# Kernel tuning notes

Hardware: AMD Instinct MI355X
Metric: run time of the kernel (lower is better)

The kernel has to match this reference:

```python
import jax, jax.numpy as jnp
import numpy as np

B, C_IN, L = 256, 4, 2048
HNODE, GLEN = 256, 24
SIGMA_CONV, SIGMA_NEU = 0.1, 0.1
DROPPROB = 0.5


def setup_inputs() -> dict:
    key = jax.random.key(0)
    ks = jax.random.split(key, 7)
    x = jax.random.normal(ks[0], (B, C_IN, L), dtype=jnp.float32)
    wConv = SIGMA_CONV * jax.random.normal(ks[1], (HNODE, C_IN, GLEN), dtype=jnp.float32)
    wRect = -jax.random.normal(ks[2], (HNODE,), dtype=jnp.float32)
    wHidden = 0.3 * jax.random.normal(ks[3], (2 * HNODE, 2 * HNODE), dtype=jnp.float32)
    wHiddenBias = 0.3 * jax.random.normal(ks[4], (2 * HNODE,), dtype=jnp.float32)
    wNeu = SIGMA_NEU * jax.random.normal(ks[5], (2 * HNODE, 1), dtype=jnp.float32)
    wNeuBias = SIGMA_NEU * jax.random.normal(ks[6], (1,), dtype=jnp.float32)
    return {"x": x, "wConv": wConv, "wRect": wRect, "wHidden": wHidden,
            "wHiddenBias": wHiddenBias, "wNeu": wNeu, "wNeuBias": wNeuBias}


def reference(x, wConv, wRect, wHidden, wHiddenBias, wNeu, wNeuBias):
    # conv1d, stride 1, no padding: [B, HNODE, L-GLEN+1]
    conv = jax.lax.conv_general_dilated(
        x, wConv, window_strides=(1,), padding='VALID',
        dimension_numbers=('NCH', 'OIH', 'NCH'))
    rect = jnp.maximum(conv + wRect[None, :, None], 0.0)  # bias + relu-clamp
    maxPool = jnp.max(rect, axis=2)   # [B, HNODE]
    avgPool = jnp.mean(rect, axis=2)  # [B, HNODE]
    pool = jnp.concatenate([maxPool, avgPool], axis=1)  # [B, 2*HNODE]
    hid = jnp.maximum(pool @ wHidden + wHiddenBias, 0.0)
    out = DROPPROB * (hid @ wNeu) + wNeuBias  # [B, 1]
    return out
```

## Files before the change

### kernel.cpp

```cpp
#include <hip/hip_runtime.h>
#include <stdint.h>

#define CIN   4
#define LEN   2048
#define HN    256
#define GL    24
#define LOUT  2025
#define XP    2080

typedef short  s16x8 __attribute__((ext_vector_type(8)));
typedef float  f32x4 __attribute__((ext_vector_type(4)));

__device__ float g_pool[256 * 512];

static __device__ __forceinline__ uint16_t f2bf(float f) {
    union { float f; uint32_t u; } v; v.f = f;
    uint32_t u = v.u;
    return (uint16_t)((u + 0x7FFFu + ((u >> 16) & 1u)) >> 16);
}

#define SEL4(D, i) \
    ({ uint4 fu_ = {(D)[(i)], (D)[(i)+1], (D)[(i)+2], (D)[(i)+3]}; \
       __builtin_bit_cast(s16x8, fu_); })

static __device__ __forceinline__ void loadW(
    uint32_t (&E)[3][8], uint32_t (&O)[3][8],
    const uint16_t* xs, const uint16_t* xs2, const int (&abase)[3], int j)
{
    #pragma unroll
    for (int ks = 0; ks < 3; ++ks) {
        const uint4 e0 = *(const uint4*)&xs [abase[ks] + 128 * j];
        const uint4 e1 = *(const uint4*)&xs [abase[ks] + 128 * j + 8];
        const uint4 o0 = *(const uint4*)&xs2[abase[ks] + 128 * j];
        const uint4 o1 = *(const uint4*)&xs2[abase[ks] + 128 * j + 8];
        E[ks][0]=e0.x; E[ks][1]=e0.y; E[ks][2]=e0.z; E[ks][3]=e0.w;
        E[ks][4]=e1.x; E[ks][5]=e1.y; E[ks][6]=e1.z; E[ks][7]=e1.w;
        O[ks][0]=o0.x; O[ks][1]=o0.y; O[ks][2]=o0.z; O[ks][3]=o0.w;
        O[ks][4]=o1.x; O[ks][5]=o1.y; O[ks][6]=o1.z; O[ks][7]=o1.w;
    }
}

static __device__ __forceinline__ void procW(
    const uint32_t (&E)[3][8], const uint32_t (&O)[3][8],
    const s16x8 (&bfrag)[2][3], const float (&negb)[2],
    bool tail, int q, float (&rawmax)[2], float (&sums)[2])
{
    const f32x4 fzero = {0.f, 0.f, 0.f, 0.f};
    #pragma unroll
    for (int p = 0; p < 8; ++p) {
        s16x8 a0, a1, a2;
        if ((p & 1) == 0) {
            a0 = SEL4(E[0], p/2); a1 = SEL4(E[1], p/2); a2 = SEL4(E[2], p/2);
        } else {
            a0 = SEL4(O[0], (p-1)/2); a1 = SEL4(O[1], (p-1)/2); a2 = SEL4(O[2], (p-1)/2);
        }
        f32x4 acc0, acc1;
        acc0 = __builtin_amdgcn_mfma_f32_16x16x32_bf16(a0, bfrag[0][0], fzero, 0, 0, 0);
        acc1 = __builtin_amdgcn_mfma_f32_16x16x32_bf16(a0, bfrag[1][0], fzero, 0, 0, 0);
        acc0 = __builtin_amdgcn_mfma_f32_16x16x32_bf16(a1, bfrag[0][1], acc0, 0, 0, 0);
        acc1 = __builtin_amdgcn_mfma_f32_16x16x32_bf16(a1, bfrag[1][1], acc1, 0, 0, 0);
        acc0 = __builtin_amdgcn_mfma_f32_16x16x32_bf16(a2, bfrag[0][2], acc0, 0, 0, 0);
        acc1 = __builtin_amdgcn_mfma_f32_16x16x32_bf16(a2, bfrag[1][2], acc1, 0, 0, 0);

        if (!tail) {
            #pragma unroll
            for (int s = 0; s < 2; ++s) {
                const f32x4 a = (s == 0) ? acc0 : acc1;
                float t0 = fmaxf(a[0], negb[s]), t1 = fmaxf(a[1], negb[s]);
                float t2 = fmaxf(a[2], negb[s]), t3 = fmaxf(a[3], negb[s]);
                sums[s] += (t0 + t1) + (t2 + t3);
                rawmax[s] = fmaxf(fmaxf(rawmax[s], a[0]), a[1]);
                rawmax[s] = fmaxf(fmaxf(rawmax[s], a[2]), a[3]);
            }
        } else {
            #pragma unroll
            for (int s = 0; s < 2; ++s) {
                const f32x4 a = (s == 0) ? acc0 : acc1;
                #pragma unroll
                for (int r = 0; r < 4; ++r) {
                    int tpos = p + 128 * 15 + 32 * q + 8 * r;
                    float t = (tpos < LOUT) ? fmaxf(a[r], negb[s])
                                            : negb[s];
                    sums[s]   += t;
                    rawmax[s]  = fmaxf(rawmax[s], t);
                }
            }
        }
    }
}

__global__ __launch_bounds__(512) __attribute__((amdgpu_waves_per_eu(2, 2)))
void conv_pool_kernel(
    const float* __restrict__ x, const float* __restrict__ wConv,
    const float* __restrict__ wRect)
{
    __shared__ uint16_t xs [CIN * XP + 8];
    __shared__ uint16_t xs2[CIN * XP + 8];

    const int tid  = threadIdx.x;
    const int b    = blockIdx.x;
    const int lane = tid & 63;
    const int wid  = tid >> 6;
    const int n    = lane & 15;
    const int q    = lane >> 4;

    const float* xb = x + (size_t)b * (CIN * LEN);
    #pragma unroll
    for (int it = 0; it < 4; ++it) {
        int i = (tid + it * 512) * 4;
        float4 v = *(const float4*)(xb + i);
        int c = i >> 11, off = i & 2047;
        uint64_t pk =  (uint64_t)f2bf(v.x)
                    | ((uint64_t)f2bf(v.y) << 16)
                    | ((uint64_t)f2bf(v.z) << 32)
                    | ((uint64_t)f2bf(v.w) << 48);
        *(uint64_t*)&xs[c * XP + off] = pk;
    }
    if (tid < 64) {
        int c = tid >> 4, o = (tid & 15) * 2;
        *(uint32_t*)&xs[c * XP + 2048 + o] = 0u;
    }
    if (tid < 4) *(uint32_t*)&xs[CIN * XP + tid * 2] = 0u;

    s16x8 bfrag[2][3];
    float negb[2];
    #pragma unroll
    for (int s = 0; s < 2; ++s) {
        int h = wid * 32 + s * 16 + n;
        negb[s] = -wRect[h];
        #pragma unroll
        for (int ks = 0; ks < 3; ++ks) {
            int jb = ks * 4 + q;
            const float* wp_ = wConv + h * (CIN * GL) + jb * 8;
            float4 w0 = *(const float4*)(wp_);
            float4 w1 = *(const float4*)(wp_ + 4);
            s16x8 f;
            f[0]=(short)f2bf(w0.x); f[1]=(short)f2bf(w0.y);
            f[2]=(short)f2bf(w0.z); f[3]=(short)f2bf(w0.w);
            f[4]=(short)f2bf(w1.x); f[5]=(short)f2bf(w1.y);
            f[6]=(short)f2bf(w1.z); f[7]=(short)f2bf(w1.w);
            bfrag[s][ks] = f;
        }
    }

    int abase[3];
    #pragma unroll
    for (int ks = 0; ks < 3; ++ks) {
        int jb = ks * 4 + q;
        int c = jb / 3, g0 = (jb % 3) * 8;
        abase[ks] = c * XP + g0 + 8 * n;
    }

    __syncthreads();

    {
        const uint32_t* s0 = (const uint32_t*)xs;
        uint32_t*       s1 = (uint32_t*)xs2;
        #pragma unroll 1
        for (int g = tid; g < (CIN * XP) / 8; g += 512) {
            uint4 a = *(const uint4*)&s0[4 * g];
            uint32_t nx = s0[4 * g + 4];
            uint4 r;
            r.x = __builtin_amdgcn_alignbit(a.y, a.x, 16);
            r.y = __builtin_amdgcn_alignbit(a.z, a.y, 16);
            r.z = __builtin_amdgcn_alignbit(a.w, a.z, 16);
            r.w = __builtin_amdgcn_alignbit(nx,  a.w, 16);
            *(uint4*)&s1[4 * g] = r;
        }
    }
    __syncthreads();

    float rawmax[2] = {-1e30f, -1e30f};
    float sums[2]   = {0.f, 0.f};

    uint32_t EA[3][8], OA[3][8], EB[3][8], OB[3][8];
    loadW(EA, OA, xs, xs2, abase, 0);
    #pragma unroll 1
    for (int jj = 0; jj < 16; jj += 2) {
        loadW(EB, OB, xs, xs2, abase, jj + 1);
        procW(EA, OA, bfrag, negb, false, q, rawmax, sums);
        loadW(EA, OA, xs, xs2, abase, (jj + 2 < 16) ? jj + 2 : 15);
        procW(EB, OB, bfrag, negb, (jj + 1 == 15), q, rawmax, sums);
    }

    #pragma unroll
    for (int s = 0; s < 2; ++s) {
        float m  = rawmax[s], sm = sums[s];
        m  = fmaxf(m, __shfl_xor(m, 16, 64));  sm += __shfl_xor(sm, 16, 64);
        m  = fmaxf(m, __shfl_xor(m, 32, 64));  sm += __shfl_xor(sm, 32, 64);
        if (q == 0) {
            int h = wid * 32 + s * 16 + n;
            float bia = -negb[s];
            g_pool[(size_t)b * 512 + h]       = fmaxf(m + bia, 0.f);
            g_pool[(size_t)b * 512 + 256 + h] = (sm + 2048.f * bia) * (1.0f / 2025.0f);
        }
    }
}

__global__ __launch_bounds__(256, 4) void mlp_kernel(
    const float* __restrict__ wH, const float* __restrict__ bH,
    const float* __restrict__ wNeu, const float* __restrict__ wNeuB,
    float* __restrict__ out)
{
    __shared__ float pl[8][512];

    const int tid = threadIdx.x;
    const int og  = blockIdx.x & 7;
    const int bg  = blockIdx.x >> 3;
    const int o   = og * 64 + (tid & 63);
    const int wv  = tid >> 6;

    const float* ps = g_pool + (size_t)bg * 8 * 512;
    #pragma unroll
    for (int it = 0; it < 4; ++it) {
        int i = (tid + it * 256) * 4;
        *(float4*)&pl[0][i] = *(const float4*)(ps + i);
    }
    __syncthreads();

    float acc0 = 0.f, acc1 = 0.f;
    const float* prow0 = &pl[wv * 2][0];
    const float* prow1 = &pl[wv * 2 + 1][0];
    #pragma unroll 4
    for (int i = 0; i < 512; i += 4) {
        float4 p0 = *(const float4*)(prow0 + i);
        float4 p1 = *(const float4*)(prow1 + i);
        float w0 = wH[(i + 0) * 512 + o];
        float w1 = wH[(i + 1) * 512 + o];
        float w2 = wH[(i + 2) * 512 + o];
        float w3 = wH[(i + 3) * 512 + o];
        acc0 = fmaf(p0.x, w0, acc0); acc0 = fmaf(p0.y, w1, acc0);
        acc0 = fmaf(p0.z, w2, acc0); acc0 = fmaf(p0.w, w3, acc0);
        acc1 = fmaf(p1.x, w0, acc1); acc1 = fmaf(p1.y, w1, acc1);
        acc1 = fmaf(p1.z, w2, acc1); acc1 = fmaf(p1.w, w3, acc1);
    }
    float hb  = bH[o];
    float wn  = wNeu[o];
    float v0  = fmaxf(acc0 + hb, 0.f) * wn;
    float v1  = fmaxf(acc1 + hb, 0.f) * wn;
    #pragma unroll
    for (int dlt = 1; dlt < 64; dlt <<= 1) {
        v0 += __shfl_xor(v0, dlt, 64);
        v1 += __shfl_xor(v1, dlt, 64);
    }
    if ((tid & 63) == 0) {
        int b0 = bg * 8 + wv * 2;
        float bias = (og == 0) ? wNeuB[0] : 0.f;
        atomicAdd(&out[b0],     0.5f * v0 + bias);
        atomicAdd(&out[b0 + 1], 0.5f * v1 + bias);
    }
}

extern "C" void kernel_launch(void* const* d_in, const int* in_sizes, int n_in,
                              void* d_out, int out_size, void* d_ws, size_t ws_size,
                              hipStream_t stream) {
    const float* x        = (const float*)d_in[0];
    const float* wConv    = (const float*)d_in[1];
    const float* wRect    = (const float*)d_in[2];
    const float* wHidden  = (const float*)d_in[3];
    const float* wHidBias = (const float*)d_in[4];
    const float* wNeu     = (const float*)d_in[5];
    const float* wNeuBias = (const float*)d_in[6];
    float* out  = (float*)d_out;
    (void)d_ws; (void)ws_size;

    hipMemsetAsync(d_out, 0, 256 * sizeof(float), stream);
    conv_pool_kernel<<<256, 512, 0, stream>>>(x, wConv, wRect);
    mlp_kernel<<<256, 256, 0, stream>>>(wHidden, wHidBias, wNeu, wNeuBias, out);
}
```

Measured before the change: 123.4 us.

## Restructure MLP kernel to remove atomics and memset; raise MFMA wave priority

The MLP kernel now runs one 512-thread block per pair of batch rows. Its eight waves cover all 512 hidden outputs, and the partial sums are reduced in shared memory instead of through global atomicAdd. This removes the hipMemsetAsync launch and the atomics on the output. Separately, the conv kernel raises wave priority with s_setprio around the MFMA burst to favour matrix issue. The trade-off is that the MLP kernel now launches only 128 blocks, and each block reads the full wHidden matrix, so more weight traffic is spread over fewer blocks.

```diff
diff --git a/kernel.cpp b/kernel.cpp
--- a/kernel.cpp
+++ b/kernel.cpp
@@ -54,6 +54,7 @@
         } else {
             a0 = SEL4(O[0], (p-1)/2); a1 = SEL4(O[1], (p-1)/2); a2 = SEL4(O[2], (p-1)/2);
         }
+        __builtin_amdgcn_s_setprio(1);
         f32x4 acc0, acc1;
         acc0 = __builtin_amdgcn_mfma_f32_16x16x32_bf16(a0, bfrag[0][0], fzero, 0, 0, 0);
         acc1 = __builtin_amdgcn_mfma_f32_16x16x32_bf16(a0, bfrag[1][0], fzero, 0, 0, 0);
@@ -61,6 +62,7 @@
         acc1 = __builtin_amdgcn_mfma_f32_16x16x32_bf16(a1, bfrag[1][1], acc1, 0, 0, 0);
         acc0 = __builtin_amdgcn_mfma_f32_16x16x32_bf16(a2, bfrag[0][2], acc0, 0, 0, 0);
         acc1 = __builtin_amdgcn_mfma_f32_16x16x32_bf16(a2, bfrag[1][2], acc1, 0, 0, 0);
+        __builtin_amdgcn_s_setprio(0);
 
         if (!tail) {
             #pragma unroll
@@ -197,30 +199,29 @@
     }
 }
 
-__global__ __launch_bounds__(256, 4) void mlp_kernel(
+__global__ __launch_bounds__(512, 2) void mlp_kernel(
     const float* __restrict__ wH, const float* __restrict__ bH,
     const float* __restrict__ wNeu, const float* __restrict__ wNeuB,
     float* __restrict__ out)
 {
-    __shared__ float pl[8][512];
-
-    const int tid = threadIdx.x;
-    const int og  = blockIdx.x & 7;
-    const int bg  = blockIdx.x >> 3;
-    const int o   = og * 64 + (tid & 63);
-    const int wv  = tid >> 6;
-
-    const float* ps = g_pool + (size_t)bg * 8 * 512;
-    #pragma unroll
-    for (int it = 0; it < 4; ++it) {
-        int i = (tid + it * 256) * 4;
-        *(float4*)&pl[0][i] = *(const float4*)(ps + i);
+    __shared__ float pl[2][512];
+    __shared__ float part[8][2];
+
+    const int tid  = threadIdx.x;
+    const int bg   = blockIdx.x;
+    const int lane = tid & 63;
+    const int og   = tid >> 6;
+    const int o    = og * 64 + lane;
+
+    if (tid < 256) {
+        int i = tid * 4;
+        *(float4*)&pl[0][i] = *(const float4*)(g_pool + (size_t)bg * 1024 + i);
     }
     __syncthreads();
 
     float acc0 = 0.f, acc1 = 0.f;
-    const float* prow0 = &pl[wv * 2][0];
-    const float* prow1 = &pl[wv * 2 + 1][0];
+    const float* prow0 = &pl[0][0];
+    const float* prow1 = &pl[1][0];
     #pragma unroll 4
     for (int i = 0; i < 512; i += 4) {
         float4 p0 = *(const float4*)(prow0 + i);
@@ -243,11 +244,14 @@
         v0 += __shfl_xor(v0, dlt, 64);
         v1 += __shfl_xor(v1, dlt, 64);
     }
-    if ((tid & 63) == 0) {
-        int b0 = bg * 8 + wv * 2;
-        float bias = (og == 0) ? wNeuB[0] : 0.f;
-        atomicAdd(&out[b0],     0.5f * v0 + bias);
-        atomicAdd(&out[b0 + 1], 0.5f * v1 + bias);
+    if (lane == 0) { part[og][0] = v0; part[og][1] = v1; }
+    __syncthreads();
+
+    if (tid < 2) {
+        float s = 0.f;
+        #pragma unroll
+        for (int g = 0; g < 8; ++g) s += part[g][tid];
+        out[bg * 2 + tid] = 0.5f * s + wNeuB[0];
     }
 }
 
@@ -264,7 +268,6 @@
     float* out  = (float*)d_out;
     (void)d_ws; (void)ws_size;
 
-    hipMemsetAsync(d_out, 0, 256 * sizeof(float), stream);
     conv_pool_kernel<<<256, 512, 0, stream>>>(x, wConv, wRect);
-    mlp_kernel<<<256, 256, 0, stream>>>(wHidden, wHidBias, wNeu, wNeuBias, out);
-}
+    mlp_kernel<<<128, 512, 0, stream>>>(wHidden, wHidBias, wNeu, wNeuBias, out);
+}
```

Result: no change. 122.2 us (median of 2 runs) (-1.0%).
